# Performance work log

Measured on AMD Instinct MI355X. Metric: run time of the kernel, lower is better.

## Reference

```python
import jax, jax.numpy as jnp
import numpy as np

N = 50000
E = 800000


def sage_conv(x, edge_index, W_l, b_l, W_r):
    """PyG SAGEConv with mean aggregation.

    out = lin_l(mean_{j in N(i)} x_j) + lin_r(x_i)
    lin_l has bias, lin_r (root weight) has no bias.
    """
    src, dst = edge_index[0], edge_index[1]
    n = x.shape[0]
    msg_sum = jax.ops.segment_sum(x[src], dst, num_segments=n)          # [N, F]
    cnt = jax.ops.segment_sum(jnp.ones((edge_index.shape[1],), x.dtype), dst,
                              num_segments=n)                           # [N]
    mean = msg_sum / jnp.maximum(cnt, 1.0)[:, None]
    return mean @ W_l + b_l + x @ W_r


def setup_inputs() -> dict:
    key = jax.random.key(0)
    ks = jax.random.split(key, 10)
    dims = [(128, 128), (128, 128), (128, 64)]
    inp = {
        "x": jax.random.normal(ks[0], (N, 128), dtype=jnp.float32),
        "edge_index": jax.random.randint(ks[1], (2, E), 0, N, dtype=jnp.int64),
    }
    for i, (fi, fo) in enumerate(dims):
        scale = 1.0 / np.sqrt(fi)
        inp[f"W_l{i}"] = jax.random.uniform(ks[2 + 3 * i - (3 * i) % 1], (fi, fo), jnp.float32, -scale, scale)
        inp[f"b_l{i}"] = jnp.zeros((fo,), jnp.float32)
        inp[f"W_r{i}"] = jax.random.uniform(jax.random.fold_in(ks[3], i), (fi, fo), jnp.float32, -scale, scale)
        inp[f"W_l{i}"] = jax.random.uniform(jax.random.fold_in(ks[2], i), (fi, fo), jnp.float32, -scale, scale)
    return inp


def reference(x, edge_index, W_l0, b_l0, W_r0, W_l1, b_l1, W_r1, W_l2, b_l2, W_r2):
    # Layer 1 + relu (dropout identity in eval mode)
    h = jax.nn.relu(sage_conv(x, edge_index, W_l0, b_l0, W_r0))
    # Layer 2 + relu
    h = jax.nn.relu(sage_conv(h, edge_index, W_l1, b_l1, W_r1))
    # Output layer (no activation)
    return sage_conv(h, edge_index, W_l2, b_l2, W_r2)
```

## Files before the change

### kernel.cpp

```cpp
#include <hip/hip_runtime.h>

static inline int ceil_div(int a, int b) { return (a + b - 1) / b; }

typedef __attribute__((ext_vector_type(8))) short short8;
typedef __attribute__((ext_vector_type(4))) float f32x4;

__device__ __forceinline__ ushort bf16_rne(float v) {
  uint u = __float_as_uint(v);
  return (ushort)((u + 0x7FFFu + ((u >> 16) & 1u)) >> 16);
}

__device__ __forceinline__ void pack_dev(const float* __restrict__ Wl,
                                         const float* __restrict__ Wr,
                                         ushort* __restrict__ hi, int ct, int FOUT) {
  const int NCOL = 2 * FOUT;
  const int g = ct & 3;
  const int nn = (ct >> 2) % NCOL;
  const int kt = ct / (4 * NCOL);
  uint hw[4];
#pragma unroll
  for (int w = 0; w < 4; ++w) {
    uint h2[2];
#pragma unroll
    for (int t = 0; t < 2; ++t) {
      int j = 2 * w + t;
      int k = kt * 32 + g * 8 + j;
      float v = (nn < FOUT) ? Wl[k * FOUT + nn] : Wr[k * FOUT + (nn - FOUT)];
      h2[t] = (uint)bf16_rne(v);
    }
    hw[w] = h2[0] | (h2[1] << 16);
  }
  ((uint4*)hi)[ct] = make_uint4(hw[0], hw[1], hw[2], hw[3]);
}

__global__ void k_prep(const float* __restrict__ Wl0, const float* __restrict__ Wr0,
                       ushort* __restrict__ hi0,
                       const float* __restrict__ Wl1, const float* __restrict__ Wr1,
                       ushort* __restrict__ hi1,
                       const float* __restrict__ Wl2, const float* __restrict__ Wr2,
                       ushort* __restrict__ hi2,
                       const float* __restrict__ x, ushort* __restrict__ xb,
                       int* __restrict__ cnt, int* __restrict__ bflag,
                       int n, int zb) {
  const int b = blockIdx.x;
  const int tid = threadIdx.x;
  if (b < 16) {
    pack_dev(Wl0, Wr0, hi0, b * 256 + tid, 128);
  } else if (b < 32) {
    pack_dev(Wl1, Wr1, hi1, (b - 16) * 256 + tid, 128);
  } else if (b < 40) {
    pack_dev(Wl2, Wr2, hi2, (b - 32) * 256 + tid, 64);
  } else if (b < 40 + zb) {
    int b2 = b - 40;
    int i0 = b2 * 2048 + tid;
#pragma unroll
    for (int j = 0; j < 8; ++j) {
      int i = i0 + j * 256;
      if (i < n) cnt[i] = 0;
    }
    if (b2 == 0 && tid < 32) bflag[tid] = 0;
  } else {
    int i = (b - 40 - zb) * 256 + tid;
    if (i < n * 16) {
      const float4* ip = (const float4*)(x + (size_t)i * 8);
      float4 a = ip[0], bb = ip[1];
      uint p0 = (uint)bf16_rne(a.x) | ((uint)bf16_rne(a.y) << 16);
      uint p1 = (uint)bf16_rne(a.z) | ((uint)bf16_rne(a.w) << 16);
      uint p2 = (uint)bf16_rne(bb.x) | ((uint)bf16_rne(bb.y) << 16);
      uint p3 = (uint)bf16_rne(bb.z) | ((uint)bf16_rne(bb.w) << 16);
      ((uint4*)xb)[i] = make_uint4(p0, p1, p2, p3);
    }
  }
}


__global__ void k_count_rank(const int* __restrict__ dst, int* __restrict__ cnt,
                             ushort* __restrict__ rank, int e) {
  int i0 = (blockIdx.x * blockDim.x + threadIdx.x) * 4;
  if (i0 >= e) return;
  int d[4], r[4];
  if (i0 + 3 < e) {
    int4 dv = *(const int4*)(dst + i0);
    d[0] = dv.x; d[1] = dv.y; d[2] = dv.z; d[3] = dv.w;
  } else {
#pragma unroll
    for (int j = 0; j < 4; ++j) d[j] = (i0 + j < e) ? dst[i0 + j] : 0;
  }
#pragma unroll
  for (int j = 0; j < 4; ++j)
    if (i0 + j < e) r[j] = atomicAdd(&cnt[d[j]], 1);
  if (i0 + 3 < e) {
    ushort4 rv;
    rv.x = (ushort)r[0]; rv.y = (ushort)r[1];
    rv.z = (ushort)r[2]; rv.w = (ushort)r[3];
    *(ushort4*)(rank + i0) = rv;
  } else {
#pragma unroll
    for (int j = 0; j < 4; ++j)
      if (i0 + j < e) rank[i0 + j] = (ushort)r[j];
  }
}

#define SCAN_BS 256
#define SCAN_VPT 8
#define SCAN_CHUNK (SCAN_BS * SCAN_VPT)

__global__ __launch_bounds__(SCAN_BS) void k_scan_lb(const int* __restrict__ cnt,
                                                     int* __restrict__ row_ptr,
                                                     float* __restrict__ inv,
                                                     int* __restrict__ bflag,
                                                     int n, int nblocks) {
  __shared__ int s[SCAN_BS];
  __shared__ int s_prev;
  const int tid = threadIdx.x;
  const int bid = blockIdx.x;
  const int i0 = bid * SCAN_CHUNK + tid * SCAN_VPT;
  int v[SCAN_VPT], cv[SCAN_VPT];
  int sum = 0;
#pragma unroll
  for (int j = 0; j < SCAN_VPT; ++j) {
    int i = i0 + j;
    int c = (i < n) ? cnt[i] : 0;
    cv[j] = c;
    v[j] = sum;
    sum += c;
  }
  s[tid] = sum;
  __syncthreads();
  for (int off = 1; off < SCAN_BS; off <<= 1) {
    int t = (tid >= off) ? s[tid - off] : 0;
    __syncthreads();
    s[tid] += t;
    __syncthreads();
  }
  const int btotal = s[SCAN_BS - 1];
  if (tid == 0) {
    atomicExch(&bflag[bid], btotal + 1);
    int prev = 0;
    for (int b = 0; b < bid; ++b) {
      int f;
      do { f = atomicAdd(&bflag[b], 0); } while (f == 0);
      prev += f - 1;
    }
    s_prev = prev;
    if (bid == nblocks - 1) row_ptr[n] = prev + btotal;
  }
  __syncthreads();
  const int excl = s_prev + s[tid] - sum;
#pragma unroll
  for (int j = 0; j < SCAN_VPT; ++j) {
    int i = i0 + j;
    if (i < n) {
      row_ptr[i] = excl + v[j];
      inv[i] = 1.0f / (float)(cv[j] > 1 ? cv[j] : 1);
    }
  }
}

__global__ void k_place(const int* __restrict__ src, const int* __restrict__ dst,
                        const ushort* __restrict__ rank, const int* __restrict__ row_ptr,
                        ushort* __restrict__ csr16, int e) {
  int i0 = (blockIdx.x * blockDim.x + threadIdx.x) * 4;
  if (i0 >= e) return;
  if (i0 + 3 < e) {
    int4 dv = *(const int4*)(dst + i0);
    int4 sv = *(const int4*)(src + i0);
    ushort4 rv = *(const ushort4*)(rank + i0);
    int p0 = row_ptr[dv.x], p1 = row_ptr[dv.y], p2 = row_ptr[dv.z], p3 = row_ptr[dv.w];
    csr16[p0 + rv.x] = (ushort)sv.x;
    csr16[p1 + rv.y] = (ushort)sv.y;
    csr16[p2 + rv.z] = (ushort)sv.z;
    csr16[p3 + rv.w] = (ushort)sv.w;
  } else {
#pragma unroll
    for (int j = 0; j < 4; ++j) {
      int i = i0 + j;
      if (i < e) csr16[row_ptr[dst[i]] + rank[i]] = (ushort)src[i];
    }
  }
}

template <int FOUT>
__global__ __launch_bounds__(256) void k_gemm2b(const ushort* __restrict__ Hb,
                                                const ushort* __restrict__ Whi,
                                                const float* __restrict__ bias,
                                                ushort* __restrict__ Zb,
                                                ushort* __restrict__ Rb, int n) {
  constexpr int NCOL = 2 * FOUT;
  constexpr int NT = NCOL / 64;
  constexpr int MT = 2;
  __shared__ uint4 sA[32 * 16];

  const int tid = threadIdx.x;
  const int lane = tid & 63;
  const int wave = tid >> 6;
  const int row0 = blockIdx.x * 32;

  const int n0 = wave * (NCOL / 4);
  const int g16 = lane >> 4;
  const int l16 = lane & 15;

#pragma unroll
  for (int c = tid; c < 512; c += 256) {
    int srow = c >> 4, col16 = c & 15;
    int g = row0 + srow;
    uint4 v = make_uint4(0u, 0u, 0u, 0u);
    if (g < n) v = *(const uint4*)(Hb + (size_t)g * 128 + col16 * 8);
    sA[srow * 16 + (col16 ^ (srow & 7))] = v;
  }

  short8 bh[NT], bhN[NT];
#pragma unroll
  for (int nt = 0; nt < NT; ++nt) {
    size_t chunk = (size_t)(0 * NCOL + n0 + nt * 16 + l16) * 4 + g16;
    bh[nt] = *(const short8*)(Whi + chunk * 8);
  }
  __syncthreads();

  f32x4 acc[MT][NT];
#pragma unroll
  for (int mt = 0; mt < MT; ++mt)
#pragma unroll
    for (int nt = 0; nt < NT; ++nt) acc[mt][nt] = (f32x4)(0.f);

#pragma unroll
  for (int kt = 0; kt < 4; ++kt) {
    short8 a[MT];
#pragma unroll
    for (int mt = 0; mt < MT; ++mt) {
      int row = mt * 16 + l16;
      int slot = (kt * 4 + g16) ^ (row & 7);
      a[mt] = *(const short8*)&sA[row * 16 + slot];
    }
    if (kt < 3) {
#pragma unroll
      for (int nt = 0; nt < NT; ++nt) {
        size_t chunk = (size_t)((kt + 1) * NCOL + n0 + nt * 16 + l16) * 4 + g16;
        bhN[nt] = *(const short8*)(Whi + chunk * 8);
      }
    }
#pragma unroll
    for (int mt = 0; mt < MT; ++mt)
#pragma unroll
      for (int nt = 0; nt < NT; ++nt)
        acc[mt][nt] = __builtin_amdgcn_mfma_f32_16x16x32_bf16(a[mt], bh[nt], acc[mt][nt], 0, 0, 0);
    if (kt < 3) {
#pragma unroll
      for (int nt = 0; nt < NT; ++nt) bh[nt] = bhN[nt];
    }
  }

#pragma unroll
  for (int nt = 0; nt < NT; ++nt) {
    int col = n0 + nt * 16 + l16;
    bool isR = col >= FOUT;
    int cw = isR ? col - FOUT : col;
    float badd = isR ? bias[cw] : 0.f;
    ushort* base = isR ? Rb : Zb;
#pragma unroll
    for (int mt = 0; mt < MT; ++mt) {
#pragma unroll
      for (int j = 0; j < 4; ++j) {
        int row = row0 + mt * 16 + g16 * 4 + j;
        if (row < n) base[(size_t)row * FOUT + cw] = bf16_rne(acc[mt][nt][j] + badd);
      }
    }
  }
}

template <int FOUT, bool RELU, bool OUTB>
__global__ __launch_bounds__(256) void k_agg2(const ushort* __restrict__ Zb,
                                              const ushort* __restrict__ Rb,
                                              const int* __restrict__ row_ptr,
                                              const ushort* __restrict__ csr16,
                                              const float* __restrict__ inv,
                                              void* __restrict__ outp, int n) {
  constexpr int FL = FOUT / 8;
  constexpr int EG = 64 / FL;
  constexpr int DEPTH = (FL == 16) ? 8 : 4;
  const int lane = threadIdx.x & 63;
  const int node = blockIdx.x * 4 + (threadIdx.x >> 6);
  if (node >= n) return;
  const int c = lane % FL;
  const int eg = lane / FL;

  const int e0 = row_ptr[node];
  const int m = row_ptr[node + 1] - e0;
  const uint4* Z4 = (const uint4*)Zb;

  float acc[8];
#pragma unroll
  for (int k = 0; k < 8; ++k) acc[k] = 0.f;

  int t = eg;
  while (t < m) {
    int ss[DEPTH];
#pragma unroll
    for (int j = 0; j < DEPTH; ++j) {
      int tj = t + j * EG;
      int tc = (tj < m) ? tj : (m - 1);
      ss[j] = csr16[e0 + tc];
    }
    uint4 z[DEPTH];
#pragma unroll
    for (int j = 0; j < DEPTH; ++j) z[j] = Z4[(size_t)ss[j] * FL + c];
#pragma unroll
    for (int j = 0; j < DEPTH; ++j) {
      if (t + j * EG < m) {
        const uint* zw = (const uint*)&z[j];
#pragma unroll
        for (int w = 0; w < 4; ++w) {
          acc[2 * w]     += __uint_as_float(zw[w] << 16);
          acc[2 * w + 1] += __uint_as_float(zw[w] & 0xFFFF0000u);
        }
      }
    }
    t += DEPTH * EG;
  }

#pragma unroll
  for (int off = FL; off < 64; off <<= 1) {
#pragma unroll
    for (int k = 0; k < 8; ++k) acc[k] += __shfl_xor(acc[k], off, 64);
  }

  if (eg == 0) {
    const float iv = inv[node];
    uint4 rw = ((const uint4*)Rb)[(size_t)node * FL + c];
    const uint* rp = (const uint*)&rw;
    float o[8];
#pragma unroll
    for (int w = 0; w < 4; ++w) {
      o[2 * w]     = fmaf(acc[2 * w],     iv, __uint_as_float(rp[w] << 16));
      o[2 * w + 1] = fmaf(acc[2 * w + 1], iv, __uint_as_float(rp[w] & 0xFFFF0000u));
    }
    if (RELU) {
#pragma unroll
      for (int k = 0; k < 8; ++k) o[k] = fmaxf(o[k], 0.f);
    }
    if (OUTB) {
      uint p[4];
#pragma unroll
      for (int w = 0; w < 4; ++w)
        p[w] = (uint)bf16_rne(o[2 * w]) | ((uint)bf16_rne(o[2 * w + 1]) << 16);
      ((uint4*)outp)[(size_t)node * FL + c] = make_uint4(p[0], p[1], p[2], p[3]);
    } else {
      float4* op = (float4*)((float*)outp + (size_t)node * FOUT + c * 8);
      op[0] = make_float4(o[0], o[1], o[2], o[3]);
      op[1] = make_float4(o[4], o[5], o[6], o[7]);
    }
  }
}


extern "C" void kernel_launch(void* const* d_in, const int* in_sizes, int n_in,
                              void* d_out, int out_size, void* d_ws, size_t ws_size,
                              hipStream_t stream) {
  const float* x   = (const float*)d_in[0];
  const int*   ei  = (const int*)d_in[1];
  const float* Wl0 = (const float*)d_in[2];
  const float* bl0 = (const float*)d_in[3];
  const float* Wr0 = (const float*)d_in[4];
  const float* Wl1 = (const float*)d_in[5];
  const float* bl1 = (const float*)d_in[6];
  const float* Wr1 = (const float*)d_in[7];
  const float* Wl2 = (const float*)d_in[8];
  const float* bl2 = (const float*)d_in[9];
  const float* Wr2 = (const float*)d_in[10];
  float* out = (float*)d_out;

  const int N = in_sizes[0] / 128;
  const int E = in_sizes[1] / 2;
  const int* src = ei;
  const int* dst = ei + E;

  char* w = (char*)d_ws;
  auto alloc = [&](size_t bytes) {
    char* p = w;
    w += (bytes + 255) & ~(size_t)255;
    return p;
  };
  int*    cnt     = (int*)alloc((size_t)N * 4);
  int*    row_ptr = (int*)alloc((size_t)(N + 1) * 4);
  int*    bflag   = (int*)alloc(32 * 4);
  ushort* rank    = (ushort*)alloc((size_t)E * 2 + 256);
  ushort* csr16   = (ushort*)alloc((size_t)E * 2 + 256);
  float*  inv     = (float*)alloc((size_t)N * 4);
  ushort* Whi0    = (ushort*)alloc((size_t)4 * 256 * 4 * 16);
  ushort* Whi1    = (ushort*)alloc((size_t)4 * 256 * 4 * 16);
  ushort* Whi2    = (ushort*)alloc((size_t)4 * 128 * 4 * 16);
  ushort* XB      = (ushort*)alloc((size_t)N * 128 * 2);
  ushort* BZ      = (ushort*)alloc((size_t)N * 128 * 2);
  ushort* BRb     = (ushort*)alloc((size_t)N * 128 * 2);
  ushort* B0      = (ushort*)alloc((size_t)N * 128 * 2);
  (void)ws_size; (void)n_in; (void)out_size;

  const int ZB = ceil_div(N, 2048);
  const int PS = ceil_div(N, SCAN_CHUNK);
  const int PREP_B = 40 + ZB + ceil_div(N * 16, 256);

  k_prep<<<PREP_B, 256, 0, stream>>>(Wl0, Wr0, Whi0, Wl1, Wr1, Whi1,
                                     Wl2, Wr2, Whi2, x, XB, cnt, bflag, N, ZB);

  k_count_rank<<<ceil_div(E, 1024), 256, 0, stream>>>(dst, cnt, rank, E);
  k_scan_lb<<<PS, SCAN_BS, 0, stream>>>(cnt, row_ptr, inv, bflag, N, PS);
  k_place<<<ceil_div(E, 1024), 256, 0, stream>>>(src, dst, rank, row_ptr, csr16, E);

  k_gemm2b<128><<<ceil_div(N, 32), 256, 0, stream>>>(XB, Whi0, bl0, BZ, BRb, N);
  k_agg2<128, true, true><<<ceil_div(N, 4), 256, 0, stream>>>(BZ, BRb, row_ptr, csr16, inv, B0, N);

  k_gemm2b<128><<<ceil_div(N, 32), 256, 0, stream>>>(B0, Whi1, bl1, BZ, BRb, N);
  k_agg2<128, true, true><<<ceil_div(N, 4), 256, 0, stream>>>(BZ, BRb, row_ptr, csr16, inv, B0, N);

  k_gemm2b<64><<<ceil_div(N, 32), 256, 0, stream>>>(B0, Whi2, bl2, BZ, BRb, N);
  k_agg2<64, false, false><<<ceil_div(N, 4), 256, 0, stream>>>(BZ, BRb, row_ptr, csr16, inv, out, N);
}
```

Before: 213.2 us.

## Make GEMM persistent with LDS-resident weights and prefetched next row tile

The GEMM kernel becomes a persistent grid-stride loop: each block loads the whole packed weight matrix into shared memory once, then processes row tiles while prefetching the next tile's activations into registers. The weight packing layout changes to column-major chunks so LDS reads are contiguous. The aim is to cut repeated global weight loads and overlap activation loads with MFMA work. The aggregation kernel also issues its root-term load before the neighbor loop. In exchange, LDS use rises (64KB for FOUT=128), which limits occupancy, and each tile now needs two block barriers.

```diff
diff --git a/kernel.cpp b/kernel.cpp
--- a/kernel.cpp
+++ b/kernel.cpp
@@ -14,9 +14,10 @@
                                          const float* __restrict__ Wr,
                                          ushort* __restrict__ hi, int ct, int FOUT) {
   const int NCOL = 2 * FOUT;
-  const int g = ct & 3;
-  const int nn = (ct >> 2) % NCOL;
-  const int kt = ct / (4 * NCOL);
+  const int col = ct % NCOL;
+  const int kg = ct / NCOL;
+  const int g = kg & 3;
+  const int kt = kg >> 2;
   uint hw[4];
 #pragma unroll
   for (int w = 0; w < 4; ++w) {
@@ -25,7 +26,7 @@
     for (int t = 0; t < 2; ++t) {
       int j = 2 * w + t;
       int k = kt * 32 + g * 8 + j;
-      float v = (nn < FOUT) ? Wl[k * FOUT + nn] : Wr[k * FOUT + (nn - FOUT)];
+      float v = (col < FOUT) ? Wl[k * FOUT + col] : Wr[k * FOUT + (col - FOUT)];
       h2[t] = (uint)bf16_rne(v);
     }
     hw[w] = h2[0] | (h2[1] << 16);
@@ -181,7 +182,7 @@
 }
 
 template <int FOUT>
-__global__ __launch_bounds__(256) void k_gemm2b(const ushort* __restrict__ Hb,
+__global__ __launch_bounds__(256) void k_gemm2p(const ushort* __restrict__ Hb,
                                                 const ushort* __restrict__ Whi,
                                                 const float* __restrict__ bias,
                                                 ushort* __restrict__ Zb,
@@ -189,83 +190,112 @@
   constexpr int NCOL = 2 * FOUT;
   constexpr int NT = NCOL / 64;
   constexpr int MT = 2;
+  constexpr int WCH = NCOL * 16;
+  __shared__ uint4 sW[WCH];
   __shared__ uint4 sA[32 * 16];
 
   const int tid = threadIdx.x;
   const int lane = tid & 63;
   const int wave = tid >> 6;
-  const int row0 = blockIdx.x * 32;
-
   const int n0 = wave * (NCOL / 4);
   const int g16 = lane >> 4;
   const int l16 = lane & 15;
-
-#pragma unroll
-  for (int c = tid; c < 512; c += 256) {
-    int srow = c >> 4, col16 = c & 15;
-    int g = row0 + srow;
-    uint4 v = make_uint4(0u, 0u, 0u, 0u);
-    if (g < n) v = *(const uint4*)(Hb + (size_t)g * 128 + col16 * 8);
-    sA[srow * 16 + (col16 ^ (srow & 7))] = v;
-  }
-
-  short8 bh[NT], bhN[NT];
-#pragma unroll
-  for (int nt = 0; nt < NT; ++nt) {
-    size_t chunk = (size_t)(0 * NCOL + n0 + nt * 16 + l16) * 4 + g16;
-    bh[nt] = *(const short8*)(Whi + chunk * 8);
+  const int TILES = (n + 31) >> 5;
+  const int GRIDN = gridDim.x;
+
+  const uint4* Wg = (const uint4*)Whi;
+#pragma unroll
+  for (int i = tid; i < WCH; i += 256) sW[i] = Wg[i];
+
+  {
+    int tile = blockIdx.x;
+    if (tile < TILES) {
+      int row0 = tile * 32;
+#pragma unroll
+      for (int c = tid; c < 512; c += 256) {
+        int srow = c >> 4, col16 = c & 15;
+        int g = row0 + srow;
+        uint4 v = make_uint4(0u, 0u, 0u, 0u);
+        if (g < n) v = *(const uint4*)(Hb + (size_t)g * 128 + col16 * 8);
+        sA[srow * 16 + (col16 ^ (srow & 7))] = v;
+      }
+    }
   }
   __syncthreads();
 
-  f32x4 acc[MT][NT];
-#pragma unroll
-  for (int mt = 0; mt < MT; ++mt)
-#pragma unroll
-    for (int nt = 0; nt < NT; ++nt) acc[mt][nt] = (f32x4)(0.f);
-
-#pragma unroll
-  for (int kt = 0; kt < 4; ++kt) {
-    short8 a[MT];
-#pragma unroll
-    for (int mt = 0; mt < MT; ++mt) {
-      int row = mt * 16 + l16;
-      int slot = (kt * 4 + g16) ^ (row & 7);
-      a[mt] = *(const short8*)&sA[row * 16 + slot];
-    }
-    if (kt < 3) {
+  const float badd0 = bias[(n0 + l16) % FOUT];
+
+  for (int tile = blockIdx.x; tile < TILES; tile += GRIDN) {
+    const int row0 = tile * 32;
+    const int ntile = tile + GRIDN;
+    const bool havenext = ntile < TILES;
+
+    uint4 rr[2];
+    if (havenext) {
+      int nrow0 = ntile * 32;
+#pragma unroll
+      for (int k = 0; k < 2; ++k) {
+        int c = tid + k * 256;
+        int g = nrow0 + (c >> 4);
+        rr[k] = make_uint4(0u, 0u, 0u, 0u);
+        if (g < n) rr[k] = *(const uint4*)(Hb + (size_t)g * 128 + (c & 15) * 8);
+      }
+    }
+
+    f32x4 acc[MT][NT];
+#pragma unroll
+    for (int mt = 0; mt < MT; ++mt)
+#pragma unroll
+      for (int nt = 0; nt < NT; ++nt) acc[mt][nt] = (f32x4)(0.f);
+
+#pragma unroll
+    for (int kt = 0; kt < 4; ++kt) {
+      short8 a[MT];
+#pragma unroll
+      for (int mt = 0; mt < MT; ++mt) {
+        int row = mt * 16 + l16;
+        int slot = (kt * 4 + g16) ^ (row & 7);
+        a[mt] = *(const short8*)&sA[row * 16 + slot];
+      }
 #pragma unroll
       for (int nt = 0; nt < NT; ++nt) {
-        size_t chunk = (size_t)((kt + 1) * NCOL + n0 + nt * 16 + l16) * 4 + g16;
-        bhN[nt] = *(const short8*)(Whi + chunk * 8);
-      }
-    }
-#pragma unroll
-    for (int mt = 0; mt < MT; ++mt)
-#pragma unroll
-      for (int nt = 0; nt < NT; ++nt)
-        acc[mt][nt] = __builtin_amdgcn_mfma_f32_16x16x32_bf16(a[mt], bh[nt], acc[mt][nt], 0, 0, 0);
-    if (kt < 3) {
-#pragma unroll
-      for (int nt = 0; nt < NT; ++nt) bh[nt] = bhN[nt];
-    }
-  }
-
-#pragma unroll
-  for (int nt = 0; nt < NT; ++nt) {
-    int col = n0 + nt * 16 + l16;
-    bool isR = col >= FOUT;
-    int cw = isR ? col - FOUT : col;
-    float badd = isR ? bias[cw] : 0.f;
-    ushort* base = isR ? Rb : Zb;
-#pragma unroll
-    for (int mt = 0; mt < MT; ++mt) {
-#pragma unroll
-      for (int j = 0; j < 4; ++j) {
-        int row = row0 + mt * 16 + g16 * 4 + j;
-        if (row < n) base[(size_t)row * FOUT + cw] = bf16_rne(acc[mt][nt][j] + badd);
-      }
-    }
-  }
+        short8 b = *(const short8*)&sW[(kt * 4 + g16) * NCOL + n0 + nt * 16 + l16];
+#pragma unroll
+        for (int mt = 0; mt < MT; ++mt)
+          acc[mt][nt] = __builtin_amdgcn_mfma_f32_16x16x32_bf16(a[mt], b, acc[mt][nt], 0, 0, 0);
+      }
+    }
+
+    __syncthreads();
+
+    if (havenext) {
+#pragma unroll
+      for (int k = 0; k < 2; ++k) {
+        int c = tid + k * 256;
+        sA[(c >> 4) * 16 + ((c & 15) ^ ((c >> 4) & 7))] = rr[k];
+      }
+    }
+
+#pragma unroll
+    for (int nt = 0; nt < NT; ++nt) {
+      int col = n0 + nt * 16 + l16;
+      bool isR = col >= FOUT;
+      int cw = isR ? col - FOUT : col;
+      float badd = isR ? bias[cw] : 0.f;
+      ushort* base = isR ? Rb : Zb;
+#pragma unroll
+      for (int mt = 0; mt < MT; ++mt) {
+#pragma unroll
+        for (int j = 0; j < 4; ++j) {
+          int row = row0 + mt * 16 + g16 * 4 + j;
+          if (row < n) base[(size_t)row * FOUT + cw] = bf16_rne(acc[mt][nt][j] + badd);
+        }
+      }
+    }
+
+    __syncthreads();
+  }
+  (void)badd0;
 }
 
 template <int FOUT, bool RELU, bool OUTB>
@@ -288,6 +318,9 @@
   const int m = row_ptr[node + 1] - e0;
   const uint4* Z4 = (const uint4*)Zb;
 
+  uint4 rw = make_uint4(0u, 0u, 0u, 0u);
+  if (eg == 0) rw = ((const uint4*)Rb)[(size_t)node * FL + c];
+
   float acc[8];
 #pragma unroll
   for (int k = 0; k < 8; ++k) acc[k] = 0.f;
@@ -326,7 +359,6 @@
 
   if (eg == 0) {
     const float iv = inv[node];
-    uint4 rw = ((const uint4*)Rb)[(size_t)node * FL + c];
     const uint* rp = (const uint*)&rw;
     float o[8];
 #pragma unroll
@@ -398,6 +430,9 @@
   const int ZB = ceil_div(N, 2048);
   const int PS = ceil_div(N, SCAN_CHUNK);
   const int PREP_B = 40 + ZB + ceil_div(N * 16, 256);
+  const int TILES = ceil_div(N, 32);
+  const int G128 = (TILES < 512) ? TILES : 512;
+  const int G64  = (TILES < 1024) ? TILES : 1024;
 
   k_prep<<<PREP_B, 256, 0, stream>>>(Wl0, Wr0, Whi0, Wl1, Wr1, Whi1,
                                      Wl2, Wr2, Whi2, x, XB, cnt, bflag, N, ZB);
@@ -406,12 +441,12 @@
   k_scan_lb<<<PS, SCAN_BS, 0, stream>>>(cnt, row_ptr, inv, bflag, N, PS);
   k_place<<<ceil_div(E, 1024), 256, 0, stream>>>(src, dst, rank, row_ptr, csr16, E);
 
-  k_gemm2b<128><<<ceil_div(N, 32), 256, 0, stream>>>(XB, Whi0, bl0, BZ, BRb, N);
+  k_gemm2p<128><<<G128, 256, 0, stream>>>(XB, Whi0, bl0, BZ, BRb, N);
   k_agg2<128, true, true><<<ceil_div(N, 4), 256, 0, stream>>>(BZ, BRb, row_ptr, csr16, inv, B0, N);
 
-  k_gemm2b<128><<<ceil_div(N, 32), 256, 0, stream>>>(B0, Whi1, bl1, BZ, BRb, N);
+  k_gemm2p<128><<<G128, 256, 0, stream>>>(B0, Whi1, bl1, BZ, BRb, N);
   k_agg2<128, true, true><<<ceil_div(N, 4), 256, 0, stream>>>(BZ, BRb, row_ptr, csr16, inv, B0, N);
 
-  k_gemm2b<64><<<ceil_div(N, 32), 256, 0, stream>>>(B0, Whi2, bl2, BZ, BRb, N);
+  k_gemm2p<64><<<G64, 256, 0, stream>>>(B0, Whi2, bl2, BZ, BRb, N);
   k_agg2<64, false, false><<<ceil_div(N, 4), 256, 0, stream>>>(BZ, BRb, row_ptr, csr16, inv, out, N);
 }
```

Result: slower. 233.1 us (+9.3%).
